# Kernel optimization log

Measured on AMD Instinct MI355X. Metric: run time of the kernel, lower is better.

Reference implementation:

```python
import jax, jax.numpy as jnp
import numpy as np

DIM = 384
NUM_HEADS = 12
WIN = 7
N = WIN * WIN  # 49
B = 4096


def _relative_position_index():
    coords = np.stack(np.meshgrid(np.arange(WIN), np.arange(WIN), indexing='ij'))  # (2,W,W)
    cf = coords.reshape(2, -1)  # (2, N)
    rel = cf[:, :, None] - cf[:, None, :]  # (2, N, N)
    rel = rel.transpose(1, 2, 0).astype(np.int64)  # (N, N, 2)
    rel[:, :, 0] += WIN - 1
    rel[:, :, 1] += WIN - 1
    rel[:, :, 0] *= 2 * WIN - 1
    return jnp.asarray(rel.sum(-1), dtype=jnp.int32)  # (N, N)


def setup_inputs() -> dict:
    key = jax.random.key(0)
    ks = jax.random.split(key, 6)
    x = jax.random.normal(ks[0], (B, N, DIM), dtype=jnp.float32)
    mask = jnp.zeros((B, N, N), dtype=jnp.float32)
    qkv_w = jax.random.normal(ks[1], (3 * DIM, DIM), dtype=jnp.float32) * 0.02
    qkv_b = jnp.zeros((3 * DIM,), dtype=jnp.float32)
    proj_w = jax.random.normal(ks[2], (DIM, DIM), dtype=jnp.float32) * 0.02
    proj_b = jnp.zeros((DIM,), dtype=jnp.float32)
    bias_table = jax.random.normal(ks[3], ((2 * WIN - 1) ** 2, NUM_HEADS), dtype=jnp.float32) * 0.02
    rel_index = _relative_position_index()
    return {"x": x, "mask": mask, "qkv_w": qkv_w, "qkv_b": qkv_b,
            "proj_w": proj_w, "proj_b": proj_b, "bias_table": bias_table,
            "rel_index": rel_index}


def reference(x, mask, qkv_w, qkv_b, proj_w, proj_b, bias_table, rel_index):
    B_, n, C = x.shape
    H = NUM_HEADS
    d = C // H
    scale = d ** (-0.5)
    # fused qkv projection: (B_, n, 3, H, d)
    qkv = (x @ qkv_w.T + qkv_b).reshape(B_, n, 3, H, d)
    qkv = jnp.transpose(qkv, (2, 0, 3, 1, 4))  # (3, B_, H, n, d)
    q, k, v = qkv[0], qkv[1], qkv[2]
    attn = jnp.einsum('bhnd,bhmd->bhnm', q * scale, k)  # (B_, H, n, n)
    # relative position bias gather: (n, n, H) -> (H, n, n)
    rel_bias = jnp.transpose(bias_table[rel_index], (2, 0, 1))
    attn = attn + rel_bias[None] + mask[:, None]
    attn = jax.nn.softmax(attn, axis=-1)
    out = jnp.einsum('bhnm,bhmd->bnhd', attn, v).reshape(B_, n, C)
    return out @ proj_w.T + proj_b
```

## Files before the change

kernel.cpp:

```cpp
#include <hip/hip_runtime.h>
#include <hip/hip_bf16.h>

#define NWIN   4096
#define NTOK   49
#define CDIM   384
#define NHEAD  12
#define QKVN   1152

typedef __attribute__((ext_vector_type(8))) short bf16x8;
typedef __attribute__((ext_vector_type(4))) short bf16x4;
typedef __attribute__((ext_vector_type(4))) float f32x4;
typedef __attribute__((ext_vector_type(2))) unsigned int u32x2;
typedef unsigned int u32;
typedef unsigned short u16;

static __device__ __forceinline__ u16 f2bf(float f) {
  union { float f; u32 u; } w; w.f = f;
  u32 r = w.u + 0x7fffu + ((w.u >> 16) & 1u);
  return (u16)(r >> 16);
}
static __device__ __forceinline__ float blo(u32 v) {
  union { u32 u; float f; } w; w.u = v << 16; return w.f;
}
static __device__ __forceinline__ float bhi(u32 v) {
  union { u32 u; float f; } w; w.u = v & 0xffff0000u; return w.f;
}
static __device__ __forceinline__ u32 cvtpk2(float lo, float hi) {
  u32 r; asm("v_cvt_pk_bf16_f32 %0, %1, %2" : "=v"(r) : "v"(lo), "v"(hi));
  return r;
}
static __device__ __forceinline__ void gld_lds16(const u16* g, u16* l) {
  __builtin_amdgcn_global_load_lds((const __attribute__((address_space(1))) u32*)g,
                                   (__attribute__((address_space(3))) u32*)l, 16, 0, 0);
}

__global__ void k_prep(const float* __restrict__ qkv_w, const float* __restrict__ proj_w,
                       const float* __restrict__ btab, const int* __restrict__ ridx,
                       u16* __restrict__ wq, u16* __restrict__ wp, u32* __restrict__ rbp)
{
  const int n1 = QKVN * CDIM;
  const int n2 = CDIM * CDIM;
  const int n3 = NHEAD * NTOK * 26;
  for (int i = blockIdx.x * blockDim.x + threadIdx.x; i < n1 + n2 + n3;
       i += gridDim.x * blockDim.x) {
    if (i < n1) {
      wq[i] = f2bf(qkv_w[i]);
    } else if (i < n1 + n2) {
      wp[i - n1] = f2bf(proj_w[i - n1]);
    } else {
      int t = i - n1 - n2;
      int h = t / (NTOK * 26); int rem = t % (NTOK * 26);
      int r = rem / 26, p = rem % 26;
      float lo = 0.f, hi = 0.f;
      if (p < 25) {
        lo = btab[ridx[r * NTOK + 2 * p] * NHEAD + h];
        if (2 * p + 1 < NTOK) hi = btab[ridx[r * NTOK + 2 * p + 1] * NHEAD + h];
      }
      rbp[(h * NTOK + r) * 26 + p] = (u32)f2bf(lo) | ((u32)f2bf(hi) << 16);
    }
  }
}

__global__ void k_convx(const float* __restrict__ x, u16* __restrict__ xb, long n8)
{
  long i = (long)blockIdx.x * blockDim.x + threadIdx.x;
  long stride = (long)gridDim.x * blockDim.x;
  for (; i < n8; i += stride) {
    const float4* p = (const float4*)x + i * 2;
    float4 a = p[0], b = p[1];
    u32 w0 = (u32)f2bf(a.x) | ((u32)f2bf(a.y) << 16);
    u32 w1 = (u32)f2bf(a.z) | ((u32)f2bf(a.w) << 16);
    u32 w2 = (u32)f2bf(b.x) | ((u32)f2bf(b.y) << 16);
    u32 w3 = (u32)f2bf(b.z) | ((u32)f2bf(b.w) << 16);
    uint4 v; v.x = w0; v.y = w1; v.z = w2; v.w = w3;
    ((uint4*)xb)[i] = v;
  }
}

template<bool OUT_BF16>
__global__ __launch_bounds__(256, 4)
void k_gemm(const u16* __restrict__ A, int lda,
            const u16* __restrict__ Bt, const float* __restrict__ bias,
            void* __restrict__ C, int ldc, int K, int tiles_n)
{
  __shared__ alignas(16) u16 As[128 * 64];
  __shared__ alignas(16) u16 Bs[128 * 64];
  const int tid = threadIdx.x;
  const int w = tid >> 6, l = tid & 63;

  const int nwg = (int)gridDim.x;
  const int xcd = (int)blockIdx.x & 7, idx8 = (int)blockIdx.x >> 3;
  const int q8 = nwg >> 3, r8w = nwg & 7;
  const int lid = (xcd < r8w ? xcd * (q8 + 1) : r8w * (q8 + 1) + (xcd - r8w) * q8) + idx8;

  const int tm = lid / tiles_n, tn = lid % tiles_n;
  const int wm = (w >> 1) * 64, wn = (w & 1) * 64;
  const long arow0 = (long)tm * 128;
  const long brow0 = (long)tn * 128;
  const int r8 = l >> 3;
  const int c8 = ((l & 7) ^ r8) * 8;

  f32x4 acc[4][4];
  const f32x4 z = {0.f, 0.f, 0.f, 0.f};
#pragma unroll
  for (int m = 0; m < 4; ++m)
#pragma unroll
    for (int n = 0; n < 4; ++n) acc[m][n] = z;

  for (int kk = 0; kk < K; kk += 64) {
    __syncthreads();
#pragma unroll
    for (int q = 0; q < 4; ++q) {
      int ra = w * 32 + q * 8;
      gld_lds16(A  + (arow0 + ra + r8) * (long)lda + kk + c8, &As[ra * 64]);
      gld_lds16(Bt + (brow0 + ra + r8) * (long)K   + kk + c8, &Bs[ra * 64]);
    }
    __syncthreads();
#pragma unroll
    for (int ks = 0; ks < 2; ++ks) {
      const int ko = ks * 32 + (l >> 4) * 8;
      const int rl = l & 15;
      const int sa = (rl & 7) * 8;
      bf16x8 af[4], bfr[4];
#pragma unroll
      for (int m = 0; m < 4; ++m) af[m]  = *(const bf16x8*)&As[(wm + m * 16 + rl) * 64 + (ko ^ sa)];
#pragma unroll
      for (int n = 0; n < 4; ++n) bfr[n] = *(const bf16x8*)&Bs[(wn + n * 16 + rl) * 64 + (ko ^ sa)];
#pragma unroll
      for (int m = 0; m < 4; ++m)
#pragma unroll
        for (int n = 0; n < 4; ++n)
          acc[m][n] = __builtin_amdgcn_mfma_f32_16x16x32_bf16(bfr[n], af[m], acc[m][n], 0, 0, 0);
    }
  }

  const int li = l & 15, g4 = (l >> 4) * 4;
  float4 bv[4];
#pragma unroll
  for (int n = 0; n < 4; ++n)
    bv[n] = *(const float4*)&bias[tn * 128 + wn + n * 16 + g4];
#pragma unroll
  for (int m = 0; m < 4; ++m) {
    const long row = arow0 + wm + m * 16 + li;
#pragma unroll
    for (int n = 0; n < 4; ++n) {
      const long colb = brow0 + wn + n * 16 + g4;
      float v0 = acc[m][n][0] + bv[n].x;
      float v1 = acc[m][n][1] + bv[n].y;
      float v2 = acc[m][n][2] + bv[n].z;
      float v3 = acc[m][n][3] + bv[n].w;
      if (OUT_BF16) {
        u32x2 pk;
        pk[0] = (u32)f2bf(v0) | ((u32)f2bf(v1) << 16);
        pk[1] = (u32)f2bf(v2) | ((u32)f2bf(v3) << 16);
        *(u32x2*)((u16*)C + row * ldc + colb) = pk;
      } else {
        float4 pk; pk.x = v0; pk.y = v1; pk.z = v2; pk.w = v3;
        *(float4*)((float*)C + row * ldc + colb) = pk;
      }
    }
  }
}

__global__ __launch_bounds__(256, 4)
void k_attn(u16* __restrict__ qkv, const float* __restrict__ maskc,
            const u32* __restrict__ rbp)
{
  __shared__ alignas(16) u16 Vt[4][32 * 64];
  __shared__ alignas(16) u32 mp[NTOK * 26];
  const int tid = threadIdx.x;
  const int w = tid >> 6, l = tid & 63;
  const int g = l >> 4, li = l & 15;
  const int id = blockIdx.x;
  const int logical = (id & 7) * ((int)gridDim.x >> 3) + (id >> 3);
  const int bl = logical / 3, hg = logical - bl * 3;
  const int h = hg * 4 + w;
  const long rowbase = (long)bl * NTOK;
  const float scale = 0.17677669529663687f;

  bf16x8 kf[4];
#pragma unroll
  for (int jm = 0; jm < 4; ++jm) {
    int rj = jm * 16 + li; if (rj >= NTOK) rj = NTOK - 1;
    kf[jm] = *(const bf16x8*)(qkv + (rowbase + rj) * QKVN + CDIM + h * 32 + g * 8);
  }
  bf16x8 qfc = *(const bf16x8*)(qkv + (rowbase + li) * QKVN + h * 32 + g * 8);

  u16* vt = Vt[w];
  {
    const int jj = l >> 2;
    const int d0 = (l & 3) * 8;
#pragma unroll
    for (int it = 0; it < 4; ++it) {
      int j = it * 16 + jj;
      bf16x8 vv = {0, 0, 0, 0, 0, 0, 0, 0};
      if (j < NTOK)
        vv = *(const bf16x8*)(qkv + (rowbase + j) * QKVN + 2 * CDIM + h * 32 + d0);
#pragma unroll
      for (int t = 0; t < 8; ++t)
        vt[(d0 + t) * 64 + (j ^ (t << 3))] = (u16)vv[t];
    }
  }
  for (int e = tid; e < NTOK * 25; e += 256) {
    int i = e / 25, p = e - i * 25;
    const float* mrow = maskc + (long)bl * (NTOK * NTOK) + i * NTOK;
    float lo = mrow[2 * p];
    float hi = (2 * p + 1 < NTOK) ? mrow[2 * p + 1] : 0.f;
    mp[i * 26 + p] = (u32)f2bf(lo) | ((u32)f2bf(hi) << 16);
  }
  if (tid < NTOK) mp[tid * 26 + 25] = 0;
  __syncthreads();

  const int sw = (li & 7) << 3;
  const f32x4 z = {0.f, 0.f, 0.f, 0.f};
  f32x4 oacc[4][2];
#pragma unroll
  for (int im = 0; im < 4; ++im)
#pragma unroll
    for (int dn = 0; dn < 2; ++dn) oacc[im][dn] = z;

#pragma unroll
  for (int in = 0; in < 4; ++in) {
    __builtin_amdgcn_s_setprio(1);
    f32x4 s[4];
#pragma unroll
    for (int jm = 0; jm < 4; ++jm)
      s[jm] = __builtin_amdgcn_mfma_f32_16x16x32_bf16(kf[jm], qfc, z, 0, 0, 0);
    __builtin_amdgcn_s_setprio(0);

    bf16x8 qfn = qfc;
    if (in < 3) {
      int ri = (in + 1) * 16 + li; if (ri >= NTOK) ri = NTOK - 1;
      qfn = *(const bf16x8*)(qkv + (rowbase + ri) * QKVN + h * 32 + g * 8);
    }

    const int i = 16 * in + li;
    const int ic = i < NTOK ? i : NTOK - 1;
#pragma unroll
    for (int jm = 0; jm < 4; ++jm) {
      int p0 = 8 * jm + 2 * g; if (p0 > 24) p0 = 24;
      const u32* bp = rbp + (h * NTOK + ic) * 26 + p0;
      u32 b0w = bp[0], b1w = bp[1];
      u32 m0w = mp[ic * 26 + p0], m1w = mp[ic * 26 + p0 + 1];
      s[jm][0] = s[jm][0] * scale + blo(b0w) + blo(m0w);
      s[jm][1] = s[jm][1] * scale + bhi(b0w) + bhi(m0w);
      s[jm][2] = s[jm][2] * scale + blo(b1w) + blo(m1w);
      s[jm][3] = s[jm][3] * scale + bhi(b1w) + bhi(m1w);
    }

    float mx = -3.0e38f;
#pragma unroll
    for (int jm = 0; jm < 4; ++jm)
#pragma unroll
      for (int rr = 0; rr < 4; ++rr) mx = fmaxf(mx, s[jm][rr]);
    mx = fmaxf(mx, __shfl_xor(mx, 16));
    mx = fmaxf(mx, __shfl_xor(mx, 32));
    float sum = 0.f;
#pragma unroll
    for (int jm = 0; jm < 4; ++jm) {
      const int j0 = 16 * jm + 4 * g;
#pragma unroll
      for (int rr = 0; rr < 4; ++rr) {
        float p = (j0 + rr < NTOK) ? __expf(s[jm][rr] - mx) : 0.f;
        s[jm][rr] = p; sum += p;
      }
    }
    sum += __shfl_xor(sum, 16);
    sum += __shfl_xor(sum, 32);
    const float inv = (i < NTOK) ? (1.f / sum) : 0.f;

    __builtin_amdgcn_s_setprio(1);
#pragma unroll
    for (int ks = 0; ks < 2; ++ks) {
      union { u32 ww[4]; bf16x8 v8; } pa;
      pa.ww[0] = cvtpk2(s[2 * ks][0] * inv, s[2 * ks][1] * inv);
      pa.ww[1] = cvtpk2(s[2 * ks][2] * inv, s[2 * ks][3] * inv);
      pa.ww[2] = cvtpk2(s[2 * ks + 1][0] * inv, s[2 * ks + 1][1] * inv);
      pa.ww[3] = cvtpk2(s[2 * ks + 1][2] * inv, s[2 * ks + 1][3] * inv);
#pragma unroll
      for (int dn = 0; dn < 2; ++dn) {
        union { bf16x4 hh[2]; bf16x8 v8; } vfr;
        const u16* vrow = &vt[(16 * dn + li) * 64];
        vfr.hh[0] = *(const bf16x4*)&vrow[(32 * ks + 4 * g) ^ sw];
        vfr.hh[1] = *(const bf16x4*)&vrow[(32 * ks + 16 + 4 * g) ^ sw];
        oacc[in][dn] = __builtin_amdgcn_mfma_f32_16x16x32_bf16(pa.v8, vfr.v8, oacc[in][dn], 0, 0, 0);
      }
    }
    __builtin_amdgcn_s_setprio(0);
    qfc = qfn;
  }

#pragma unroll
  for (int im = 0; im < 4; ++im) {
#pragma unroll
    for (int rr = 0; rr < 4; ++rr) {
      const int i = 16 * im + 4 * g + rr;
      if (i < NTOK) {
        u16* orow = qkv + (rowbase + i) * QKVN + h * 32;
#pragma unroll
        for (int dn = 0; dn < 2; ++dn)
          orow[16 * dn + li] = f2bf(oacc[im][dn][rr]);
      }
    }
  }
}

extern "C" void kernel_launch(void* const* d_in, const int* in_sizes, int n_in,
                              void* d_out, int out_size, void* d_ws, size_t ws_size,
                              hipStream_t stream)
{
  const float* x      = (const float*)d_in[0];
  const float* mask   = (const float*)d_in[1];
  const float* qkv_w  = (const float*)d_in[2];
  const float* qkv_b  = (const float*)d_in[3];
  const float* proj_w = (const float*)d_in[4];
  const float* proj_b = (const float*)d_in[5];
  const float* btab   = (const float*)d_in[6];
  const int*   ridx   = (const int*)d_in[7];
  float* out = (float*)d_out;

  auto need = [](int bc) -> size_t {
    return (size_t)bc * NTOK * QKVN * 2
         + (size_t)bc * NTOK * CDIM * 2
         + (size_t)QKVN * CDIM * 2
         + (size_t)CDIM * CDIM * 2
         + (size_t)NHEAD * NTOK * 26 * 4
         + 1024;
  };
  int BC = NWIN;
  while (BC > 128 && need(BC) > ws_size) BC >>= 1;

  char* p = (char*)d_ws;
  u16* qkvbuf = (u16*)p;  p += (size_t)BC * NTOK * QKVN * 2;
  u16* xb     = (u16*)p;  p += (size_t)BC * NTOK * CDIM * 2;
  u16* wq     = (u16*)p;  p += (size_t)QKVN * CDIM * 2;
  u16* wp     = (u16*)p;  p += (size_t)CDIM * CDIM * 2;
  u32* rbp    = (u32*)p;

  k_prep<<<512, 256, 0, stream>>>(qkv_w, proj_w, btab, ridx, wq, wp, rbp);

  const int nc = NWIN / BC;
  const int Mc = BC * NTOK;
  for (int c = 0; c < nc; ++c) {
    const float* xc = x + (size_t)c * Mc * CDIM;
    k_convx<<<2048, 256, 0, stream>>>(xc, xb, (long)Mc * CDIM / 8);
    k_gemm<true><<<(Mc / 128) * 9, 256, 0, stream>>>(
        xb, CDIM, wq, qkv_b, (void*)qkvbuf, QKVN, CDIM, 9);
    k_attn<<<BC * 3, 256, 0, stream>>>(
        qkvbuf, mask + (size_t)c * BC * NTOK * NTOK, rbp);
    k_gemm<false><<<(Mc / 128) * 3, 256, 0, stream>>>(
        qkvbuf, QKVN, wp, proj_b, (void*)(out + (size_t)c * Mc * CDIM), CDIM, CDIM, 3);
  }
}
```

Baseline: 715.7 us.

## Scatter QKV into per-window-head slices and prepack mask in prep kernel

The QKV GEMM epilogue now writes Q, K and V into contiguous per-(window, head) slices, so the attention kernel reads compact 49x32 blocks instead of strided rows of the 1152-wide buffer. The mask is converted to packed bf16 pairs once in the prep kernel and copied into LDS with direct global-to-LDS loads. Attention output goes to a separate 384-wide buffer (reusing xb) so the projection GEMM reads a denser A matrix. This trades extra prep work over the full mask and scattered 8-byte epilogue stores for more coalesced attention loads.

```diff
diff --git a/kernel.cpp b/kernel.cpp
--- a/kernel.cpp
+++ b/kernel.cpp
@@ -6,6 +6,8 @@
 #define CDIM   384
 #define NHEAD  12
 #define QKVN   1152
+#define SLICE  1568
+#define MPROW  28
 
 typedef __attribute__((ext_vector_type(8))) short bf16x8;
 typedef __attribute__((ext_vector_type(4))) short bf16x4;
@@ -36,18 +38,21 @@
 
 __global__ void k_prep(const float* __restrict__ qkv_w, const float* __restrict__ proj_w,
                        const float* __restrict__ btab, const int* __restrict__ ridx,
-                       u16* __restrict__ wq, u16* __restrict__ wp, u32* __restrict__ rbp)
+                       const float* __restrict__ mask,
+                       u16* __restrict__ wq, u16* __restrict__ wp, u32* __restrict__ rbp,
+                       u32* __restrict__ mpk)
 {
   const int n1 = QKVN * CDIM;
   const int n2 = CDIM * CDIM;
   const int n3 = NHEAD * NTOK * 26;
-  for (int i = blockIdx.x * blockDim.x + threadIdx.x; i < n1 + n2 + n3;
+  const int n4 = NWIN * NTOK * MPROW;
+  for (int i = blockIdx.x * blockDim.x + threadIdx.x; i < n1 + n2 + n3 + n4;
        i += gridDim.x * blockDim.x) {
     if (i < n1) {
       wq[i] = f2bf(qkv_w[i]);
     } else if (i < n1 + n2) {
       wp[i - n1] = f2bf(proj_w[i - n1]);
-    } else {
+    } else if (i < n1 + n2 + n3) {
       int t = i - n1 - n2;
       int h = t / (NTOK * 26); int rem = t % (NTOK * 26);
       int r = rem / 26, p = rem % 26;
@@ -57,6 +62,17 @@
         if (2 * p + 1 < NTOK) hi = btab[ridx[r * NTOK + 2 * p + 1] * NHEAD + h];
       }
       rbp[(h * NTOK + r) * 26 + p] = (u32)f2bf(lo) | ((u32)f2bf(hi) << 16);
+    } else {
+      int t2 = i - n1 - n2 - n3;
+      int wi = t2 / MPROW, p = t2 - wi * MPROW;
+      u32 v = 0;
+      if (p < 25) {
+        const float* mrow = mask + (long)wi * NTOK;
+        float lo = mrow[2 * p];
+        float hi = (2 * p + 1 < NTOK) ? mrow[2 * p + 1] : 0.f;
+        v = (u32)f2bf(lo) | ((u32)f2bf(hi) << 16);
+      }
+      mpk[t2] = v;
     }
   }
 }
@@ -77,7 +93,7 @@
   }
 }
 
-template<bool OUT_BF16>
+template<bool OUT_SLICE>
 __global__ __launch_bounds__(256, 4)
 void k_gemm(const u16* __restrict__ A, int lda,
             const u16* __restrict__ Bt, const float* __restrict__ bias,
@@ -141,33 +157,39 @@
     bv[n] = *(const float4*)&bias[tn * 128 + wn + n * 16 + g4];
 #pragma unroll
   for (int m = 0; m < 4; ++m) {
-    const long row = arow0 + wm + m * 16 + li;
+    const int row = (int)arow0 + wm + m * 16 + li;
+    const int b = (int)(((unsigned long long)(unsigned)row * 342393ull) >> 24);
+    const int tok = row - b * 49;
 #pragma unroll
     for (int n = 0; n < 4; ++n) {
-      const long colb = brow0 + wn + n * 16 + g4;
       float v0 = acc[m][n][0] + bv[n].x;
       float v1 = acc[m][n][1] + bv[n].y;
       float v2 = acc[m][n][2] + bv[n].z;
       float v3 = acc[m][n][3] + bv[n].w;
-      if (OUT_BF16) {
+      const int col = (int)brow0 + wn + n * 16 + g4;
+      if (OUT_SLICE) {
+        const int t = (col >= 768) ? 2 : ((col >= 384) ? 1 : 0);
+        const int rem = col - t * 384;
+        const int hh = rem >> 5, d = rem & 31;
+        const long dst = (((long)b * NHEAD + hh) * 3 + t) * SLICE + tok * 32 + d;
         u32x2 pk;
         pk[0] = (u32)f2bf(v0) | ((u32)f2bf(v1) << 16);
         pk[1] = (u32)f2bf(v2) | ((u32)f2bf(v3) << 16);
-        *(u32x2*)((u16*)C + row * ldc + colb) = pk;
+        *(u32x2*)((u16*)C + dst) = pk;
       } else {
         float4 pk; pk.x = v0; pk.y = v1; pk.z = v2; pk.w = v3;
-        *(float4*)((float*)C + row * ldc + colb) = pk;
+        *(float4*)((float*)C + (long)row * ldc + col) = pk;
       }
     }
   }
 }
 
 __global__ __launch_bounds__(256, 4)
-void k_attn(u16* __restrict__ qkv, const float* __restrict__ maskc,
-            const u32* __restrict__ rbp)
+void k_attn(const u16* __restrict__ qkv, u16* __restrict__ ob,
+            const u32* __restrict__ mpk, const u32* __restrict__ rbp)
 {
   __shared__ alignas(16) u16 Vt[4][32 * 64];
-  __shared__ alignas(16) u32 mp[NTOK * 26];
+  __shared__ alignas(16) u32 mp[1536];
   const int tid = threadIdx.x;
   const int w = tid >> 6, l = tid & 63;
   const int g = l >> 4, li = l & 15;
@@ -178,13 +200,18 @@
   const long rowbase = (long)bl * NTOK;
   const float scale = 0.17677669529663687f;
 
+  const long sb = ((long)bl * NHEAD + h) * 3 * SLICE;
+  const u16* qs = qkv + sb;
+  const u16* ks = qs + SLICE;
+  const u16* vs = qs + 2 * SLICE;
+
   bf16x8 kf[4];
 #pragma unroll
   for (int jm = 0; jm < 4; ++jm) {
     int rj = jm * 16 + li; if (rj >= NTOK) rj = NTOK - 1;
-    kf[jm] = *(const bf16x8*)(qkv + (rowbase + rj) * QKVN + CDIM + h * 32 + g * 8);
-  }
-  bf16x8 qfc = *(const bf16x8*)(qkv + (rowbase + li) * QKVN + h * 32 + g * 8);
+    kf[jm] = *(const bf16x8*)(ks + rj * 32 + g * 8);
+  }
+  bf16x8 qfc = *(const bf16x8*)(qs + li * 32 + g * 8);
 
   u16* vt = Vt[w];
   {
@@ -195,20 +222,20 @@
       int j = it * 16 + jj;
       bf16x8 vv = {0, 0, 0, 0, 0, 0, 0, 0};
       if (j < NTOK)
-        vv = *(const bf16x8*)(qkv + (rowbase + j) * QKVN + 2 * CDIM + h * 32 + d0);
+        vv = *(const bf16x8*)(vs + j * 32 + d0);
 #pragma unroll
       for (int t = 0; t < 8; ++t)
         vt[(d0 + t) * 64 + (j ^ (t << 3))] = (u16)vv[t];
     }
   }
-  for (int e = tid; e < NTOK * 25; e += 256) {
-    int i = e / 25, p = e - i * 25;
-    const float* mrow = maskc + (long)bl * (NTOK * NTOK) + i * NTOK;
-    float lo = mrow[2 * p];
-    float hi = (2 * p + 1 < NTOK) ? mrow[2 * p + 1] : 0.f;
-    mp[i * 26 + p] = (u32)f2bf(lo) | ((u32)f2bf(hi) << 16);
-  }
-  if (tid < NTOK) mp[tid * 26 + 25] = 0;
+  {
+    const u32* mpkb = mpk + (long)bl * (NTOK * MPROW);
+    for (int base = w * 1024; base < NTOK * MPROW * 4; base += 4096) {
+      int soff = base + l * 16;
+      if (soff > NTOK * MPROW * 4 - 16) soff = NTOK * MPROW * 4 - 16;
+      gld_lds16((const u16*)((const char*)mpkb + soff), (u16*)((char*)mp + base));
+    }
+  }
   __syncthreads();
 
   const int sw = (li & 7) << 3;
@@ -231,7 +258,7 @@
     bf16x8 qfn = qfc;
     if (in < 3) {
       int ri = (in + 1) * 16 + li; if (ri >= NTOK) ri = NTOK - 1;
-      qfn = *(const bf16x8*)(qkv + (rowbase + ri) * QKVN + h * 32 + g * 8);
+      qfn = *(const bf16x8*)(qs + ri * 32 + g * 8);
     }
 
     const int i = 16 * in + li;
@@ -241,7 +268,7 @@
       int p0 = 8 * jm + 2 * g; if (p0 > 24) p0 = 24;
       const u32* bp = rbp + (h * NTOK + ic) * 26 + p0;
       u32 b0w = bp[0], b1w = bp[1];
-      u32 m0w = mp[ic * 26 + p0], m1w = mp[ic * 26 + p0 + 1];
+      u32 m0w = mp[ic * MPROW + p0], m1w = mp[ic * MPROW + p0 + 1];
       s[jm][0] = s[jm][0] * scale + blo(b0w) + blo(m0w);
       s[jm][1] = s[jm][1] * scale + bhi(b0w) + bhi(m0w);
       s[jm][2] = s[jm][2] * scale + blo(b1w) + blo(m1w);
@@ -271,18 +298,18 @@
 
     __builtin_amdgcn_s_setprio(1);
 #pragma unroll
-    for (int ks = 0; ks < 2; ++ks) {
+    for (int ks2 = 0; ks2 < 2; ++ks2) {
       union { u32 ww[4]; bf16x8 v8; } pa;
-      pa.ww[0] = cvtpk2(s[2 * ks][0] * inv, s[2 * ks][1] * inv);
-      pa.ww[1] = cvtpk2(s[2 * ks][2] * inv, s[2 * ks][3] * inv);
-      pa.ww[2] = cvtpk2(s[2 * ks + 1][0] * inv, s[2 * ks + 1][1] * inv);
-      pa.ww[3] = cvtpk2(s[2 * ks + 1][2] * inv, s[2 * ks + 1][3] * inv);
+      pa.ww[0] = cvtpk2(s[2 * ks2][0] * inv, s[2 * ks2][1] * inv);
+      pa.ww[1] = cvtpk2(s[2 * ks2][2] * inv, s[2 * ks2][3] * inv);
+      pa.ww[2] = cvtpk2(s[2 * ks2 + 1][0] * inv, s[2 * ks2 + 1][1] * inv);
+      pa.ww[3] = cvtpk2(s[2 * ks2 + 1][2] * inv, s[2 * ks2 + 1][3] * inv);
 #pragma unroll
       for (int dn = 0; dn < 2; ++dn) {
         union { bf16x4 hh[2]; bf16x8 v8; } vfr;
         const u16* vrow = &vt[(16 * dn + li) * 64];
-        vfr.hh[0] = *(const bf16x4*)&vrow[(32 * ks + 4 * g) ^ sw];
-        vfr.hh[1] = *(const bf16x4*)&vrow[(32 * ks + 16 + 4 * g) ^ sw];
+        vfr.hh[0] = *(const bf16x4*)&vrow[(32 * ks2 + 4 * g) ^ sw];
+        vfr.hh[1] = *(const bf16x4*)&vrow[(32 * ks2 + 16 + 4 * g) ^ sw];
         oacc[in][dn] = __builtin_amdgcn_mfma_f32_16x16x32_bf16(pa.v8, vfr.v8, oacc[in][dn], 0, 0, 0);
       }
     }
@@ -296,7 +323,7 @@
     for (int rr = 0; rr < 4; ++rr) {
       const int i = 16 * im + 4 * g + rr;
       if (i < NTOK) {
-        u16* orow = qkv + (rowbase + i) * QKVN + h * 32;
+        u16* orow = ob + (rowbase + i) * CDIM + h * 32;
 #pragma unroll
         for (int dn = 0; dn < 2; ++dn)
           orow[16 * dn + li] = f2bf(oacc[im][dn][rr]);
@@ -319,13 +346,13 @@
   const int*   ridx   = (const int*)d_in[7];
   float* out = (float*)d_out;
 
-  auto need = [](int bc) -> size_t {
+  const size_t fixed = (size_t)QKVN * CDIM * 2 + (size_t)CDIM * CDIM * 2
+                     + (size_t)NHEAD * NTOK * 26 * 4
+                     + (size_t)NWIN * NTOK * MPROW * 4 + 1024;
+  auto need = [&](int bc) -> size_t {
     return (size_t)bc * NTOK * QKVN * 2
          + (size_t)bc * NTOK * CDIM * 2
-         + (size_t)QKVN * CDIM * 2
-         + (size_t)CDIM * CDIM * 2
-         + (size_t)NHEAD * NTOK * 26 * 4
-         + 1024;
+         + fixed;
   };
   int BC = NWIN;
   while (BC > 128 && need(BC) > ws_size) BC >>= 1;
@@ -335,9 +362,10 @@
   u16* xb     = (u16*)p;  p += (size_t)BC * NTOK * CDIM * 2;
   u16* wq     = (u16*)p;  p += (size_t)QKVN * CDIM * 2;
   u16* wp     = (u16*)p;  p += (size_t)CDIM * CDIM * 2;
-  u32* rbp    = (u32*)p;
-
-  k_prep<<<512, 256, 0, stream>>>(qkv_w, proj_w, btab, ridx, wq, wp, rbp);
+  u32* rbp    = (u32*)p;  p += (size_t)NHEAD * NTOK * 26 * 4;
+  u32* mpk    = (u32*)p;
+
+  k_prep<<<512, 256, 0, stream>>>(qkv_w, proj_w, btab, ridx, mask, wq, wp, rbp, mpk);
 
   const int nc = NWIN / BC;
   const int Mc = BC * NTOK;
@@ -347,8 +375,8 @@
     k_gemm<true><<<(Mc / 128) * 9, 256, 0, stream>>>(
         xb, CDIM, wq, qkv_b, (void*)qkvbuf, QKVN, CDIM, 9);
     k_attn<<<BC * 3, 256, 0, stream>>>(
-        qkvbuf, mask + (size_t)c * BC * NTOK * NTOK, rbp);
+        qkvbuf, xb, mpk + (size_t)c * BC * NTOK * MPROW, rbp);
     k_gemm<false><<<(Mc / 128) * 3, 256, 0, stream>>>(
-        qkvbuf, QKVN, wp, proj_b, (void*)(out + (size_t)c * Mc * CDIM), CDIM, CDIM, 3);
-  }
-}
+        xb, CDIM, wp, proj_b, (void*)(out + (size_t)c * Mc * CDIM), CDIM, CDIM, 3);
+  }
+}
```

After: 685.5 us (median of 2 runs). -4.2%, faster.
